# Optimization experiments

Measured on AMD Instinct MI355X. Metric: run time of the kernel, lower is better.

Reference implementation:

```python
import jax, jax.numpy as jnp
import numpy as np

N, K, H, E, HEADS, MULT = 10000, 32, 128, 128, 8, 2
HD = H // HEADS


def _ln(x, g, b):
    m = jnp.mean(x, axis=-1, keepdims=True)
    v = jnp.var(x, axis=-1, keepdims=True)
    return (x - m) * jax.lax.rsqrt(v + 1e-5) * g + b


def setup_inputs() -> dict:
    key = jax.random.key(0)
    ks = jax.random.split(key, 40)
    s = 0.05
    inp = {
        "node_features": jax.random.normal(ks[0], (N, H), jnp.float32),
        "edge_features": jax.random.normal(ks[1], (N, K, H), jnp.float32),
        "edge_attr": jax.random.normal(ks[2], (N, K, E), jnp.float32),
        "neighbor_list": jax.random.randint(ks[3], (N, K), 0, N),
        "num_valid": jax.random.randint(ks[4], (N,), 1, K + 1),
        # edge_linear: E -> H (with activation)
        "W_edge": jax.random.normal(ks[5], (E, H), jnp.float32) * s,
        "b_edge": jnp.zeros((H,), jnp.float32),
        # node_linear: 2H -> H (cat of center + gathered neighbor features)
        "W_node": jax.random.normal(ks[6], (2 * H, H), jnp.float32) * s,
        "b_node": jnp.zeros((H,), jnp.float32),
        # message_linear: 2H -> H
        "W_msg": jax.random.normal(ks[7], (2 * H, H), jnp.float32) * s,
        "b_msg": jnp.zeros((H,), jnp.float32),
        # multi-head attention in/out projections
        "W_qkv": jax.random.normal(ks[8], (H, 3 * H), jnp.float32) * s,
        "b_qkv": jnp.zeros((3 * H,), jnp.float32),
        "W_out": jax.random.normal(ks[9], (H, H), jnp.float32) * s,
        "b_out": jnp.zeros((H,), jnp.float32),
        # layernorms
        "g_attn": jnp.ones((H,), jnp.float32), "be_attn": jnp.zeros((H,), jnp.float32),
        "g_fn": jnp.ones((H,), jnp.float32), "be_fn": jnp.zeros((H,), jnp.float32),
        "g_fe": jnp.ones((H,), jnp.float32), "be_fe": jnp.zeros((H,), jnp.float32),
        # FFNs (node and edge), hidden = MULT*H
        "Wn1": jax.random.normal(ks[10], (H, MULT * H), jnp.float32) * s,
        "bn1": jnp.zeros((MULT * H,), jnp.float32),
        "Wn2": jax.random.normal(ks[11], (MULT * H, H), jnp.float32) * s,
        "bn2": jnp.zeros((H,), jnp.float32),
        "We1": jax.random.normal(ks[12], (H, MULT * H), jnp.float32) * s,
        "be1": jnp.zeros((MULT * H,), jnp.float32),
        "We2": jax.random.normal(ks[13], (MULT * H, H), jnp.float32) * s,
        "be2": jnp.zeros((H,), jnp.float32),
    }
    return inp


def _block(node_features, edge_features, edge_attr, neighbor_list, mask,
           W_edge, b_edge, W_node, b_node, W_msg, b_msg,
           W_qkv, b_qkv, W_out, b_out,
           g_attn, be_attn, g_fn, be_fn, g_fe, be_fe,
           Wn1, bn1, Wn2, bn2, We1, be1, We2, be2):
    act = jax.nn.gelu
    # --- pre-attention norm on nodes ---
    node_hidden = _ln(node_features, g_attn, be_attn)                 # [N,H]
    # --- graph attention: gather -> MLPs -> local windowed attention -> scatter ---
    edge_hidden = act(jnp.einsum('nke,eh->nkh', edge_attr, W_edge) + b_edge)   # [N,K,H]
    nbr = node_hidden[neighbor_list]                                   # [N,K,H] gather
    center = jnp.broadcast_to(node_hidden[:, None, :], nbr.shape)      # [N,K,H]
    node_cat = jnp.concatenate([center, nbr], axis=-1)                 # [N,K,2H]
    node_hid = act(jnp.einsum('nkf,fh->nkh', node_cat, W_node) + b_node)
    msg = act(jnp.einsum('nkf,fh->nkh',
                         jnp.concatenate([edge_hidden, node_hid], axis=-1),
                         W_msg) + b_msg)                               # [N,K,H]
    # multi-head self-attention per node over its K neighbors, key padding mask
    qkv = jnp.einsum('nkh,hf->nkf', msg, W_qkv) + b_qkv                # [N,K,3H]
    q, k, v = jnp.split(qkv, 3, axis=-1)
    q = q.reshape(N, K, HEADS, HD)
    k = k.reshape(N, K, HEADS, HD)
    v = v.reshape(N, K, HEADS, HD)
    scores = jnp.einsum('nqhd,nkhd->nhqk', q, k) / np.sqrt(HD)         # [N,heads,K,K]
    scores = jnp.where(mask[:, None, None, :], scores, jnp.float32(-1e9))
    attn = jax.nn.softmax(scores, axis=-1)
    ctx = jnp.einsum('nhqk,nkhd->nqhd', attn, v).reshape(N, K, H)
    edge_out = jnp.einsum('nkh,hf->nkf', ctx, W_out) + b_out           # [N,K,H]
    # masked scatter-aggregate back to nodes
    node_out = jnp.sum(edge_out * mask[:, :, None], axis=1)            # [N,H]
    # residuals
    node_features = node_out + node_features
    edge_features = edge_out + edge_features
    # --- FFN block ---
    nh = _ln(node_features, g_fn, be_fn)
    eh = _ln(edge_features, g_fe, be_fe)
    nh = act(nh @ Wn1 + bn1) @ Wn2 + bn2
    eh = jnp.einsum('nkf,fh->nkh', act(jnp.einsum('nkh,hf->nkf', eh, We1) + be1), We2) + be2
    return node_features + nh, edge_features + eh


def reference(node_features, edge_features, edge_attr, neighbor_list, num_valid,
              W_edge, b_edge, W_node, b_node, W_msg, b_msg,
              W_qkv, b_qkv, W_out, b_out,
              g_attn, be_attn, g_fn, be_fn, g_fe, be_fe,
              Wn1, bn1, Wn2, bn2, We1, be1, We2, be2):
    mask = jnp.arange(K)[None, :] < num_valid[:, None]                 # [N,K] bool
    return _block(node_features, edge_features, edge_attr, neighbor_list, mask,
                  W_edge, b_edge, W_node, b_node, W_msg, b_msg,
                  W_qkv, b_qkv, W_out, b_out,
                  g_attn, be_attn, g_fn, be_fn, g_fe, be_fe,
                  Wn1, bn1, Wn2, bn2, We1, be1, We2, be2)
```

## Files before the change

kernel.cpp:

```cpp
#include <hip/hip_runtime.h>
#include <hip/hip_bf16.h>
#include <cstddef>

#define N_NODES 10000
#define KNBR 32
#define HDIM 128
#define NHEADS 8

using short8 = __attribute__((ext_vector_type(8))) short;
using short4v = __attribute__((ext_vector_type(4))) short;
using f32x4 = __attribute__((ext_vector_type(4))) float;

__device__ __forceinline__ f32x4 mfma16(short8 a, short8 b, f32x4 c) {
  return __builtin_amdgcn_mfma_f32_16x16x32_bf16(a, b, c, 0, 0, 0);
}

__device__ __forceinline__ short f2bf(float f) {
  __hip_bfloat16 h = __float2bfloat16(f);
  return __builtin_bit_cast(short, h);
}
__device__ __forceinline__ float bf2f(short s) {
  unsigned u = ((unsigned)(unsigned short)s) << 16;
  return __builtin_bit_cast(float, u);
}

__device__ __forceinline__ float gelu_f(float x) {
  float u = x * fmaf(x * x, -0.1029432f, -2.3022077f);
  return x * __builtin_amdgcn_rcpf(1.0f + __builtin_amdgcn_exp2f(u));
}

__device__ __forceinline__ short4v pack4f(float a, float b, float c, float d) {
  short4v v; v[0] = f2bf(a); v[1] = f2bf(b); v[2] = f2bf(c); v[3] = f2bf(d);
  return v;
}
__device__ __forceinline__ short4v pack_gelu4(f32x4 acc, float4 bb) {
  return pack4f(gelu_f(acc[0] + bb.x), gelu_f(acc[1] + bb.y),
                gelu_f(acc[2] + bb.z), gelu_f(acc[3] + bb.w));
}

__device__ __forceinline__ short8 ld_sw128(const short* b, int r, int ch) {
  return *(const short8*)(b + r * 128 + (((ch ^ (r & 7))) << 3));
}
__device__ __forceinline__ short8 ld_sw256(const short* b, int r, int ch) {
  return *(const short8*)(b + r * 256 + (((ch ^ (r & 7))) << 3));
}
__device__ __forceinline__ void st_sw128(short* b, int r, int col, short v) {
  b[r * 128 + ((((col >> 3) ^ (r & 7))) << 3) + (col & 7)] = v;
}
__device__ __forceinline__ void st_sw128_v4(short* b, int r, int colb, short4v v) {
  *(short4v*)(b + r * 128 + ((((colb >> 3) ^ (r & 7))) << 3) + (colb & 7)) = v;
}
__device__ __forceinline__ void st_sw256_v4(short* b, int r, int colb, short4v v) {
  *(short4v*)(b + r * 256 + ((((colb >> 3) ^ (r & 7))) << 3) + (colb & 7)) = v;
}


template <int MT, int NT, int KS, typename ALoad, typename Epi>
__device__ __forceinline__ void wgemm(ALoad aload, const short* __restrict__ Bt,
                                      Epi epi) {
  const int lane = threadIdx.x & 63;
  const int lm = lane & 15, lq = lane >> 4;
#pragma unroll
  for (int nt = 0; nt < NT; ++nt) {
    short8 b[KS];
#pragma unroll
    for (int k = 0; k < KS; ++k)
      b[k] = *(const short8*)(Bt + (nt * 16 + lm) * (KS * 32) + k * 32 + lq * 8);
#pragma unroll
    for (int mt = 0; mt < MT; ++mt) {
      short8 a[KS];
#pragma unroll
      for (int k = 0; k < KS; ++k) a[k] = aload(mt * 16 + lm, k, lq);
      f32x4 acc = {0.f, 0.f, 0.f, 0.f};
#pragma unroll
      for (int k = 0; k < KS; ++k) acc = mfma16(a[k], b[k], acc);
      epi(mt, nt, acc);
    }
  }
}

template <int MT, int NT, int KS, typename ALoad, typename Epi>
__device__ __forceinline__ void wgemm_t(ALoad aload, const short* __restrict__ Bt,
                                        Epi epi) {
  const int lane = threadIdx.x & 63;
  const int lm = lane & 15, lq = lane >> 4;
#pragma unroll
  for (int nt = 0; nt < NT; ++nt) {
    short8 b[KS];
#pragma unroll
    for (int k = 0; k < KS; ++k)
      b[k] = *(const short8*)(Bt + (nt * 16 + lm) * (KS * 32) + k * 32 + lq * 8);
#pragma unroll
    for (int mt = 0; mt < MT; ++mt) {
      short8 a[KS];
#pragma unroll
      for (int k = 0; k < KS; ++k) a[k] = aload(mt * 16 + lm, k, lq);
      f32x4 acc = {0.f, 0.f, 0.f, 0.f};
#pragma unroll
      for (int k = 0; k < KS; ++k) acc = mfma16(b[k], a[k], acc);
      epi(mt, nt, acc);
    }
  }
}

template <int MT, int NT, int KS, typename ALoad>
__device__ __forceinline__ void wgemm_pass(ALoad aload,
                                           const short* __restrict__ Bt,
                                           int brs, f32x4 (&acc)[MT][NT]) {
  const int lane = threadIdx.x & 63;
  const int lm = lane & 15, lq = lane >> 4;
#pragma unroll
  for (int nt = 0; nt < NT; ++nt) {
    short8 b[KS];
#pragma unroll
    for (int k = 0; k < KS; ++k)
      b[k] = *(const short8*)(Bt + (nt * 16 + lm) * brs + k * 32 + lq * 8);
#pragma unroll
    for (int mt = 0; mt < MT; ++mt) {
      short8 a[KS];
#pragma unroll
      for (int k = 0; k < KS; ++k) a[k] = aload(mt * 16 + lm, k, lq);
#pragma unroll
      for (int k = 0; k < KS; ++k)
        acc[mt][nt] = mfma16(a[k], b[k], acc[mt][nt]);
    }
  }
}

template <int MT, int NT, int KS, typename ALoad>
__device__ __forceinline__ void wgemm_t_pass(ALoad aload,
                                             const short* __restrict__ Bt,
                                             int brs, f32x4 (&acc)[MT][NT]) {
  const int lane = threadIdx.x & 63;
  const int lm = lane & 15, lq = lane >> 4;
#pragma unroll
  for (int nt = 0; nt < NT; ++nt) {
    short8 b[KS];
#pragma unroll
    for (int k = 0; k < KS; ++k)
      b[k] = *(const short8*)(Bt + (nt * 16 + lm) * brs + k * 32 + lq * 8);
#pragma unroll
    for (int mt = 0; mt < MT; ++mt) {
      short8 a[KS];
#pragma unroll
      for (int k = 0; k < KS; ++k) a[k] = aload(mt * 16 + lm, k, lq);
#pragma unroll
      for (int k = 0; k < KS; ++k)
        acc[mt][nt] = mfma16(b[k], a[k], acc[mt][nt]);
    }
  }
}

struct WSrc { const float* p[9]; };

__global__ void wprep_kernel(WSrc ws, short* __restrict__ dst) {
  const int cum[10] = {0, 16384, 49152, 81920, 131072, 147456, 180224, 212992, 245760, 278528};
  const int Ks[9] = {128, 256, 256, 128, 128, 128, 256, 128, 256};
  const int Ns[9] = {128, 128, 128, 384, 128, 256, 128, 256, 128};
  int eg = blockIdx.x * 256 + threadIdx.x;
  int id = 0;
#pragma unroll
  for (int i = 0; i < 8; ++i) id += (eg >= cum[i + 1]) ? 1 : 0;
  int e = eg - cum[id];
  int K = Ks[id];
  int n = (K == 128) ? (e >> 7) : (e >> 8);
  int k = e - n * K;
  dst[eg] = f2bf(ws.p[id][k * Ns[id] + n]);
}

__global__ __launch_bounds__(256) void ln_in_kernel(
    const float* __restrict__ in, const float* __restrict__ g,
    const float* __restrict__ be, short* __restrict__ out) {
  __shared__ float scr[32 * 8 * 2 + 64];
  const int tid = threadIdx.x;
  const int r = tid >> 3, j = tid & 7;
  const int base = blockIdx.x * 32;
  const int rg = base + r;
  const bool valid = rg < N_NODES;
  float4 v[4];
#pragma unroll
  for (int i = 0; i < 4; ++i)
    v[i] = valid ? ((const float4*)(in + (size_t)rg * 128 + j * 16))[i]
                 : make_float4(0.f, 0.f, 0.f, 0.f);
  float s = 0.f, s2 = 0.f;
#pragma unroll
  for (int i = 0; i < 4; ++i) {
    s += v[i].x + v[i].y + v[i].z + v[i].w;
    s2 = fmaf(v[i].x, v[i].x, s2); s2 = fmaf(v[i].y, v[i].y, s2);
    s2 = fmaf(v[i].z, v[i].z, s2); s2 = fmaf(v[i].w, v[i].w, s2);
  }
  scr[r * 8 + j] = s;
  scr[256 + r * 8 + j] = s2;
  __syncthreads();
  if (tid < 32) {
    float ss = 0.f, q2 = 0.f;
#pragma unroll
    for (int i = 0; i < 8; ++i) { ss += scr[tid * 8 + i]; q2 += scr[256 + tid * 8 + i]; }
    float mn = ss * (1.f / 128.f);
    float vr = fmaf(-mn, mn, q2 * (1.f / 128.f));
    scr[512 + tid] = mn;
    scr[544 + tid] = rsqrtf(vr + 1e-5f);
  }
  __syncthreads();
  if (!valid) return;
  float mn = scr[512 + r], rs = scr[544 + r];
  short8 o[2];
#pragma unroll
  for (int i = 0; i < 4; ++i) {
    int c0 = j * 16 + i * 4;
    float4 gg = *(const float4*)(g + c0);
    float4 bb = *(const float4*)(be + c0);
    float* vf = (float*)&v[i];
    float* gf = (float*)&gg;
    float* bf = (float*)&bb;
#pragma unroll
    for (int e = 0; e < 4; ++e)
      o[i >> 1][(i & 1) * 4 + e] = f2bf(fmaf((vf[e] - mn) * rs, gf[e], bf[e]));
  }
  *(short8*)(out + (size_t)rg * 128 + j * 16) = o[0];
  *(short8*)(out + (size_t)rg * 128 + j * 16 + 8) = o[1];
}

__global__ __launch_bounds__(256, 4) void egab_main(
    const float* __restrict__ nf, const float* __restrict__ ef,
    const float* __restrict__ ea, const int* __restrict__ nlist,
    const int* __restrict__ nvalid,
    const float* __restrict__ b_edge, const float* __restrict__ b_node,
    const float* __restrict__ b_msg, const float* __restrict__ b_qkv,
    const float* __restrict__ b_out, const float* __restrict__ g_fe,
    const float* __restrict__ be_fe, const float* __restrict__ be1,
    const float* __restrict__ be2,
    const short* __restrict__ WtE, const short* __restrict__ WtN,
    const short* __restrict__ WtM, const short* __restrict__ WtQ,
    const short* __restrict__ WtO, const short* __restrict__ WtE1,
    const short* __restrict__ WtE2, const short* __restrict__ nh_bf,
    float* __restrict__ out_node, float* __restrict__ out_edge) {
  __shared__ short lds[16384];
  short* R0 = lds;
  short* R1 = lds + 4096;
  short* R2 = lds + 8192;
  short* R3 = lds + 12288;

  const int tid = threadIdx.x;
  const int w = tid >> 6;
  const int lane = tid & 63;
  const int lm = lane & 15, lq = lane >> 4;
  const int base = blockIdx.x;
  const int n0 = w * 32;

  {
    const float* eap = ea + (size_t)base * 4096;
    int r = tid >> 3;
    int sg = tid & 7;
#pragma unroll
    for (int j = 0; j < 2; ++j) {
      int ch = sg * 2 + j;
      float4 fa = ((const float4*)eap)[r * 32 + ch * 2];
      float4 fb = ((const float4*)eap)[r * 32 + ch * 2 + 1];
      short8 v = {f2bf(fa.x), f2bf(fa.y), f2bf(fa.z), f2bf(fa.w),
                  f2bf(fb.x), f2bf(fb.y), f2bf(fb.z), f2bf(fb.w)};
      *(short8*)(R0 + r * 128 + ((ch ^ (r & 7)) << 3)) = v;
    }
    int idx = nlist[base * KNBR + r];
    const short* srow = nh_bf + (size_t)idx * 128;
#pragma unroll
    for (int j = 0; j < 2; ++j) {
      int ch = sg * 2 + j;
      short8 v = *(const short8*)(srow + ch * 8);
      *(short8*)(R1 + r * 128 + ((ch ^ (r & 7)) << 3)) = v;
    }
  }
  __syncthreads();

  wgemm_t<2, 2, 4>(
      [&](int r, int k, int q) { return ld_sw128(R0, r, k * 4 + q); },
      WtE + (size_t)n0 * 128,
      [&](int mt, int nt, f32x4 acc) {
        int colb = n0 + nt * 16 + lq * 4;
        float4 bb = *(const float4*)(b_edge + colb);
        st_sw128_v4(R2, mt * 16 + lm, colb, pack_gelu4(acc, bb));
      });
  {
    f32x4 ac[2][2];
#pragma unroll
    for (int mt = 0; mt < 2; ++mt)
#pragma unroll
      for (int nt = 0; nt < 2; ++nt) ac[mt][nt] = {0.f, 0.f, 0.f, 0.f};
    wgemm_t_pass<2, 2, 4>(
        [&](int r, int k, int q) {
          (void)r;
          return *(const short8*)(nh_bf + (size_t)base * 128 + k * 32 + q * 8);
        },
        WtN + (size_t)n0 * 256, 256, ac);
    wgemm_t_pass<2, 2, 4>(
        [&](int r, int k, int q) { return ld_sw128(R1, r, k * 4 + q); },
        WtN + (size_t)n0 * 256 + 128, 256, ac);
#pragma unroll
    for (int mt = 0; mt < 2; ++mt)
#pragma unroll
      for (int nt = 0; nt < 2; ++nt) {
        int colb = n0 + nt * 16 + lq * 4;
        float4 bb = *(const float4*)(b_node + colb);
        st_sw128_v4(R3, mt * 16 + lm, colb, pack_gelu4(ac[mt][nt], bb));
      }
  }
  __syncthreads();

  {
    f32x4 ac[2][2];
#pragma unroll
    for (int mt = 0; mt < 2; ++mt)
#pragma unroll
      for (int nt = 0; nt < 2; ++nt) ac[mt][nt] = {0.f, 0.f, 0.f, 0.f};
    wgemm_t_pass<2, 2, 4>(
        [&](int r, int k, int q) { return ld_sw128(R2, r, k * 4 + q); },
        WtM + (size_t)n0 * 256, 256, ac);
    wgemm_t_pass<2, 2, 4>(
        [&](int r, int k, int q) { return ld_sw128(R3, r, k * 4 + q); },
        WtM + (size_t)n0 * 256 + 128, 256, ac);
#pragma unroll
    for (int mt = 0; mt < 2; ++mt)
#pragma unroll
      for (int nt = 0; nt < 2; ++nt) {
        int colb = n0 + nt * 16 + lq * 4;
        float4 bb = *(const float4*)(b_msg + colb);
        st_sw128_v4(R0, mt * 16 + lm, colb, pack_gelu4(ac[mt][nt], bb));
      }
  }
  __syncthreads();

  {
    const int q0 = w * 96;
    wgemm<2, 6, 4>(
        [&](int r, int k, int q) { return ld_sw128(R0, r, k * 4 + q); },
        WtQ + (size_t)q0 * 128,
        [&](int mt, int nt, f32x4 acc) {
          int c = q0 + nt * 16;
          float bb = b_qkv[c + lm];
          int m = mt * 16 + lq * 4;
          if (c < 256) {
            short* dst = (c < 128 ? R1 + ((c >> 4) * 32) * 16
                                  : R2 + (((c - 128) >> 4) * 32) * 16);
#pragma unroll
            for (int rr = 0; rr < 4; ++rr)
              dst[(m + rr) * 16 + lm] = f2bf(acc[rr] + bb);
          } else {
            int rv = (c - 256) + lm;
            short4v pv;
#pragma unroll
            for (int rr = 0; rr < 4; ++rr) pv[rr] = f2bf(acc[rr] + bb);
            int chv = m >> 3;
            *(short4v*)(R3 + rv * 32 + ((chv ^ (rv & 3)) << 3) + (m & 7)) = pv;
          }
        });
  }
  __syncthreads();

  {
    const short8 zz = {0, 0, 0, 0, 0, 0, 0, 0};
    const f32x4 z4 = {0.f, 0.f, 0.f, 0.f};
    const int nvv = nvalid[base];
#pragma unroll
    for (int it = 0; it < 2; ++it) {
      int h = (it << 2) | w;
      short* qh = R1 + h * 512;
      short* kh = R2 + h * 512;
      short8 bk[2];
#pragma unroll
      for (int nt = 0; nt < 2; ++nt)
        bk[nt] = (lq < 2) ? *(const short8*)(kh + (nt * 16 + lm) * 16 + lq * 8) : zz;
      float sc[2][2][4];
#pragma unroll
      for (int mt = 0; mt < 2; ++mt) {
        short8 aq = (lq < 2) ? *(const short8*)(qh + (mt * 16 + lm) * 16 + lq * 8) : zz;
#pragma unroll
        for (int nt = 0; nt < 2; ++nt) {
          f32x4 s = mfma16(aq, bk[nt], z4);
#pragma unroll
          for (int rr = 0; rr < 4; ++rr) {
            float x = s[rr] * 0.25f;
            if (nt * 16 + lm >= nvv) x = -1e9f;
            sc[mt][nt][rr] = x;
          }
        }
      }
#pragma unroll
      for (int mt = 0; mt < 2; ++mt)
#pragma unroll
        for (int rr = 0; rr < 4; ++rr) {
          float x0 = sc[mt][0][rr], x1 = sc[mt][1][rr];
          float mx = fmaxf(x0, x1);
          mx = fmaxf(mx, __shfl_xor(mx, 1, 16));
          mx = fmaxf(mx, __shfl_xor(mx, 2, 16));
          mx = fmaxf(mx, __shfl_xor(mx, 4, 16));
          mx = fmaxf(mx, __shfl_xor(mx, 8, 16));
          float e0 = __expf(x0 - mx), e1 = __expf(x1 - mx);
          float sm = e0 + e1;
          sm += __shfl_xor(sm, 1, 16);
          sm += __shfl_xor(sm, 2, 16);
          sm += __shfl_xor(sm, 4, 16);
          sm += __shfl_xor(sm, 8, 16);
          float ri = 1.f / sm;
          int row = mt * 16 + lq * 4 + rr;
          qh[row * 16 + lm] = f2bf(e0 * ri);
          kh[row * 16 + lm] = f2bf(e1 * ri);
        }
#pragma unroll
      for (int mt = 0; mt < 2; ++mt) {
        const short* psrc = (lq < 2) ? qh : kh;
        short8 pa = *(const short8*)(psrc + (mt * 16 + lm) * 16 + (lq & 1) * 8);
        int rv = h * 16 + lm;
        short8 vb = *(const short8*)(R3 + rv * 32 + ((lq ^ (rv & 3)) << 3));
        f32x4 c = mfma16(pa, vb, z4);
#pragma unroll
        for (int rr = 0; rr < 4; ++rr)
          st_sw128(R0, mt * 16 + lq * 4 + rr, h * 16 + lm, f2bf(c[rr]));
      }
    }
  }
  __syncthreads();

  {
    int nv = nvalid[base];
    float nsum[2] = {0.f, 0.f};
    wgemm<2, 2, 4>(
        [&](int r, int k, int q) { return ld_sw128(R0, r, k * 4 + q); },
        WtO + (size_t)n0 * 128,
        [&](int mt, int nt, f32x4 acc) {
          int col = n0 + nt * 16 + lm;
          float bb = b_out[col];
#pragma unroll
          for (int rr = 0; rr < 4; ++rr) {
            int kk = mt * 16 + lq * 4 + rr;
            float eo = acc[rr] + bb;
            if (kk < nv) nsum[nt] += eo;
            float efv = ef[((size_t)base * KNBR + kk) * 128 + col];
            st_sw128(R1, kk, col, f2bf(eo + efv));
          }
        });
#pragma unroll
    for (int nt = 0; nt < 2; ++nt) {
      float v = nsum[nt];
      v += __shfl_xor(v, 16, 64);
      v += __shfl_xor(v, 32, 64);
      if (lq == 0) {
        int col = n0 + nt * 16 + lm;
        out_node[(size_t)base * 128 + col] =
            v + nf[(size_t)base * 128 + col];
      }
    }
  }
  __syncthreads();

  {
    float* scr = (float*)R2;
    int r = tid >> 3, sg = tid & 7;
    short8 xv[2];
    float s = 0.f, s2 = 0.f;
#pragma unroll
    for (int j = 0; j < 2; ++j) {
      int ch = sg * 2 + j;
      xv[j] = *(const short8*)(R1 + r * 128 + ((ch ^ (r & 7)) << 3));
#pragma unroll
      for (int e = 0; e < 8; ++e) {
        float x = bf2f(xv[j][e]);
        s += x;
        s2 = fmaf(x, x, s2);
      }
    }
    scr[r * 8 + sg] = s;
    scr[256 + r * 8 + sg] = s2;
    __syncthreads();
    if (tid < 32) {
      float ss = 0.f, q2 = 0.f;
#pragma unroll
      for (int i = 0; i < 8; ++i) { ss += scr[tid * 8 + i]; q2 += scr[256 + tid * 8 + i]; }
      float mn = ss * (1.f / 128.f);
      float vr = fmaf(-mn, mn, q2 * (1.f / 128.f));
      scr[512 + tid * 2] = mn;
      scr[512 + tid * 2 + 1] = rsqrtf(vr + 1e-5f);
    }
    __syncthreads();
    float mn = scr[512 + r * 2], rs = scr[512 + r * 2 + 1];
#pragma unroll
    for (int j = 0; j < 2; ++j) {
      int ch = sg * 2 + j;
      int c0 = ch * 8;
      float4 g0 = *(const float4*)(g_fe + c0);
      float4 g1 = *(const float4*)(g_fe + c0 + 4);
      float4 b0 = *(const float4*)(be_fe + c0);
      float4 b1 = *(const float4*)(be_fe + c0 + 4);
      const float* gp0 = (const float*)&g0;
      const float* gp1 = (const float*)&g1;
      const float* bp0 = (const float*)&b0;
      const float* bp1 = (const float*)&b1;
      short8 ov;
#pragma unroll
      for (int e = 0; e < 4; ++e) {
        ov[e] = f2bf(fmaf((bf2f(xv[j][e]) - mn) * rs, gp0[e], bp0[e]));
        ov[4 + e] = f2bf(fmaf((bf2f(xv[j][4 + e]) - mn) * rs, gp1[e], bp1[e]));
      }
      *(short8*)(R0 + r * 128 + ((ch ^ (r & 7)) << 3)) = ov;
    }
  }
  __syncthreads();

  {
    const int f0 = w * 64;
    wgemm_t<2, 4, 4>(
        [&](int r, int k, int q) { return ld_sw128(R0, r, k * 4 + q); },
        WtE1 + (size_t)f0 * 128,
        [&](int mt, int nt, f32x4 acc) {
          int colb = f0 + nt * 16 + lq * 4;
          float4 bb = *(const float4*)(be1 + colb);
          st_sw256_v4(R2, mt * 16 + lm, colb, pack_gelu4(acc, bb));
        });
  }
  __syncthreads();

  {
    f32x4 ac[2][2];
#pragma unroll
    for (int mt = 0; mt < 2; ++mt)
#pragma unroll
      for (int nt = 0; nt < 2; ++nt) ac[mt][nt] = {0.f, 0.f, 0.f, 0.f};
    wgemm_pass<2, 2, 4>(
        [&](int r, int k, int q) { return ld_sw256(R2, r, k * 4 + q); },
        WtE2 + (size_t)n0 * 256, 256, ac);
    wgemm_pass<2, 2, 4>(
        [&](int r, int k, int q) { return ld_sw256(R2, r, 16 + k * 4 + q); },
        WtE2 + (size_t)n0 * 256 + 128, 256, ac);
#pragma unroll
    for (int mt = 0; mt < 2; ++mt)
#pragma unroll
      for (int nt = 0; nt < 2; ++nt) {
        int col = n0 + nt * 16 + lm;
        float bb = be2[col];
#pragma unroll
        for (int rr = 0; rr < 4; ++rr) {
          int m = mt * 16 + lq * 4 + rr;
          float rv = bf2f(R1[m * 128 + ((((col >> 3) ^ (m & 7))) << 3) + (col & 7)]);
          out_edge[((size_t)base * KNBR + m) * 128 + col] =
              rv + ac[mt][nt][rr] + bb;
        }
      }
  }
}

__global__ __launch_bounds__(256, 4) void node_ffn_kernel(
    const float* __restrict__ nres, const float* __restrict__ g,
    const float* __restrict__ be, const short* __restrict__ WtN1,
    const float* __restrict__ bn1, const short* __restrict__ WtN2,
    const float* __restrict__ bn2, float* __restrict__ out) {
  __shared__ short lds[8192];
  short* EHN = lds;
  float* scr = (float*)(lds + 2048);
  short* HID = lds + 4096;

  const int tid = threadIdx.x;
  const int w = tid >> 6;
  const int lane = tid & 63;
  const int lm = lane & 15, lq = lane >> 4;
  const int base = blockIdx.x * 16;
  const int n0 = w * 32;

  {
    int r = tid >> 4, sg = tid & 15;
    bool valid = (base + r) < N_NODES;
    float xf[8];
#pragma unroll
    for (int i = 0; i < 2; ++i) {
      float4 v = valid ? ((const float4*)(nres + (size_t)(base + r) * 128 + sg * 8))[i]
                       : make_float4(0.f, 0.f, 0.f, 0.f);
      xf[i * 4] = v.x; xf[i * 4 + 1] = v.y; xf[i * 4 + 2] = v.z; xf[i * 4 + 3] = v.w;
    }
    float s = 0.f, s2 = 0.f;
#pragma unroll
    for (int i = 0; i < 8; ++i) { s += xf[i]; s2 = fmaf(xf[i], xf[i], s2); }
    scr[r * 16 + sg] = s;
    scr[256 + r * 16 + sg] = s2;
    __syncthreads();
    if (tid < 16) {
      float ss = 0.f, q2 = 0.f;
#pragma unroll
      for (int i = 0; i < 16; ++i) { ss += scr[tid * 16 + i]; q2 += scr[256 + tid * 16 + i]; }
      float mn = ss * (1.f / 128.f);
      float vr = fmaf(-mn, mn, q2 * (1.f / 128.f));
      scr[512 + tid * 2] = mn;
      scr[512 + tid * 2 + 1] = rsqrtf(vr + 1e-5f);
    }
    __syncthreads();
    float mn = scr[512 + r * 2], rs = scr[512 + r * 2 + 1];
    int c0 = sg * 8;
    short8 ov;
#pragma unroll
    for (int e = 0; e < 8; ++e)
      ov[e] = f2bf(fmaf((xf[e] - mn) * rs, g[c0 + e], be[c0 + e]));
    *(short8*)(EHN + r * 128 + ((sg ^ (r & 7)) << 3)) = ov;
  }
  __syncthreads();

  {
    const int f0 = w * 64;
    wgemm_t<1, 4, 4>(
        [&](int r, int k, int q) { return ld_sw128(EHN, r, k * 4 + q); },
        WtN1 + (size_t)f0 * 128,
        [&](int mt, int nt, f32x4 acc) {
          int colb = f0 + nt * 16 + lq * 4;
          float4 bb = *(const float4*)(bn1 + colb);
          st_sw256_v4(HID, mt * 16 + lm, colb, pack_gelu4(acc, bb));
        });
  }
  __syncthreads();

  {
    f32x4 ac[1][2];
    ac[0][0] = {0.f, 0.f, 0.f, 0.f};
    ac[0][1] = {0.f, 0.f, 0.f, 0.f};
    wgemm_pass<1, 2, 4>(
        [&](int r, int k, int q) { return ld_sw256(HID, r, k * 4 + q); },
        WtN2 + (size_t)n0 * 256, 256, ac);
    wgemm_pass<1, 2, 4>(
        [&](int r, int k, int q) { return ld_sw256(HID, r, 16 + k * 4 + q); },
        WtN2 + (size_t)n0 * 256 + 128, 256, ac);
#pragma unroll
    for (int nt = 0; nt < 2; ++nt) {
      int col = n0 + nt * 16 + lm;
      float bb = bn2[col];
#pragma unroll
      for (int rr = 0; rr < 4; ++rr) {
        int m = lq * 4 + rr;
        if (base + m < N_NODES) {
          float rv = nres[(size_t)(base + m) * 128 + col];
          out[(size_t)(base + m) * 128 + col] = rv + ac[0][nt][rr] + bb;
        }
      }
    }
  }
}

extern "C" void kernel_launch(void* const* d_in, const int* in_sizes, int n_in,
                              void* d_out, int out_size, void* d_ws,
                              size_t ws_size, hipStream_t stream) {
  (void)in_sizes; (void)n_in; (void)out_size; (void)ws_size;
  const float* nf = (const float*)d_in[0];
  const float* ef = (const float*)d_in[1];
  const float* ea = (const float*)d_in[2];
  const int* nlist = (const int*)d_in[3];
  const int* nvalid = (const int*)d_in[4];
  const float* W_edge = (const float*)d_in[5];
  const float* b_edge = (const float*)d_in[6];
  const float* W_node = (const float*)d_in[7];
  const float* b_node = (const float*)d_in[8];
  const float* W_msg = (const float*)d_in[9];
  const float* b_msg = (const float*)d_in[10];
  const float* W_qkv = (const float*)d_in[11];
  const float* b_qkv = (const float*)d_in[12];
  const float* W_out = (const float*)d_in[13];
  const float* b_out = (const float*)d_in[14];
  const float* g_attn = (const float*)d_in[15];
  const float* be_attn = (const float*)d_in[16];
  const float* g_fn = (const float*)d_in[17];
  const float* be_fn = (const float*)d_in[18];
  const float* g_fe = (const float*)d_in[19];
  const float* be_fe = (const float*)d_in[20];
  const float* Wn1 = (const float*)d_in[21];
  const float* bn1 = (const float*)d_in[22];
  const float* Wn2 = (const float*)d_in[23];
  const float* bn2 = (const float*)d_in[24];
  const float* We1 = (const float*)d_in[25];
  const float* be1 = (const float*)d_in[26];
  const float* We2 = (const float*)d_in[27];
  const float* be2 = (const float*)d_in[28];

  short* ws0 = (short*)d_ws;
  short* wsW = ws0 + 1280000;
  short* WtE = wsW;
  short* WtN = wsW + 16384;
  short* WtM = wsW + 49152;
  short* WtQ = wsW + 81920;
  short* WtO = wsW + 131072;
  short* WtE1 = wsW + 147456;
  short* WtE2 = wsW + 180224;
  short* WtN1 = wsW + 212992;
  short* WtN2 = wsW + 245760;

  float* out_node = (float*)d_out;
  float* out_edge = out_node + (size_t)N_NODES * 128;

  WSrc wsrc;
  wsrc.p[0] = W_edge; wsrc.p[1] = W_node; wsrc.p[2] = W_msg;
  wsrc.p[3] = W_qkv;  wsrc.p[4] = W_out;  wsrc.p[5] = We1;
  wsrc.p[6] = We2;    wsrc.p[7] = Wn1;    wsrc.p[8] = Wn2;

  wprep_kernel<<<1088, 256, 0, stream>>>(wsrc, wsW);
  ln_in_kernel<<<(N_NODES + 31) / 32, 256, 0, stream>>>(nf, g_attn, be_attn, ws0);
  egab_main<<<N_NODES, 256, 0, stream>>>(
      nf, ef, ea, nlist, nvalid, b_edge, b_node, b_msg, b_qkv, b_out, g_fe,
      be_fe, be1, be2, WtE, WtN, WtM, WtQ, WtO, WtE1, WtE2, ws0, out_node,
      out_edge);
  node_ffn_kernel<<<(N_NODES + 15) / 16, 256, 0, stream>>>(
      out_node, g_fn, be_fn, WtN1, bn1, WtN2, bn2, out_node);
}
```

Before: 892.0 us.

## Repartition edge-kernel GEMM tiles so each wave owns one row block

Changes the per-wave work split in the fused edge kernel. Before, each of 4 waves covered all 32 edge rows and a 32-column slice. Now each wave covers 16 rows and a wider column slice, so A fragments are loaded from LDS once and reused across all N tiles, while B (weight) fragments are reloaded for each row half. The node-sum reduction now goes through an LDS partial-sum buffer plus an extra sync to combine the two row halves. The trade is fewer LDS A loads against more global or L2 weight loads and one additional barrier.

```diff
diff --git a/kernel.cpp b/kernel.cpp
--- a/kernel.cpp
+++ b/kernel.cpp
@@ -55,60 +55,57 @@
 }
 
 
-template <int MT, int NT, int KS, typename ALoad, typename Epi>
-__device__ __forceinline__ void wgemm(ALoad aload, const short* __restrict__ Bt,
-                                      Epi epi) {
+template <int NT, int KS, typename ALoad, typename Epi>
+__device__ __forceinline__ void wgemm1(int rb, ALoad aload,
+                                       const short* __restrict__ Bt, Epi epi) {
   const int lane = threadIdx.x & 63;
   const int lm = lane & 15, lq = lane >> 4;
+  short8 a[KS];
+#pragma unroll
+  for (int k = 0; k < KS; ++k) a[k] = aload(rb + lm, k, lq);
 #pragma unroll
   for (int nt = 0; nt < NT; ++nt) {
     short8 b[KS];
 #pragma unroll
     for (int k = 0; k < KS; ++k)
       b[k] = *(const short8*)(Bt + (nt * 16 + lm) * (KS * 32) + k * 32 + lq * 8);
-#pragma unroll
-    for (int mt = 0; mt < MT; ++mt) {
-      short8 a[KS];
-#pragma unroll
-      for (int k = 0; k < KS; ++k) a[k] = aload(mt * 16 + lm, k, lq);
-      f32x4 acc = {0.f, 0.f, 0.f, 0.f};
-#pragma unroll
-      for (int k = 0; k < KS; ++k) acc = mfma16(a[k], b[k], acc);
-      epi(mt, nt, acc);
-    }
-  }
-}
-
-template <int MT, int NT, int KS, typename ALoad, typename Epi>
-__device__ __forceinline__ void wgemm_t(ALoad aload, const short* __restrict__ Bt,
-                                        Epi epi) {
+    f32x4 acc = {0.f, 0.f, 0.f, 0.f};
+#pragma unroll
+    for (int k = 0; k < KS; ++k) acc = mfma16(a[k], b[k], acc);
+    epi(nt, acc);
+  }
+}
+
+template <int NT, int KS, typename ALoad, typename Epi>
+__device__ __forceinline__ void wgemm1_t(int rb, ALoad aload,
+                                         const short* __restrict__ Bt, Epi epi) {
   const int lane = threadIdx.x & 63;
   const int lm = lane & 15, lq = lane >> 4;
+  short8 a[KS];
+#pragma unroll
+  for (int k = 0; k < KS; ++k) a[k] = aload(rb + lm, k, lq);
 #pragma unroll
   for (int nt = 0; nt < NT; ++nt) {
     short8 b[KS];
 #pragma unroll
     for (int k = 0; k < KS; ++k)
       b[k] = *(const short8*)(Bt + (nt * 16 + lm) * (KS * 32) + k * 32 + lq * 8);
-#pragma unroll
-    for (int mt = 0; mt < MT; ++mt) {
-      short8 a[KS];
-#pragma unroll
-      for (int k = 0; k < KS; ++k) a[k] = aload(mt * 16 + lm, k, lq);
-      f32x4 acc = {0.f, 0.f, 0.f, 0.f};
-#pragma unroll
-      for (int k = 0; k < KS; ++k) acc = mfma16(b[k], a[k], acc);
-      epi(mt, nt, acc);
-    }
-  }
-}
-
-template <int MT, int NT, int KS, typename ALoad>
-__device__ __forceinline__ void wgemm_pass(ALoad aload,
-                                           const short* __restrict__ Bt,
-                                           int brs, f32x4 (&acc)[MT][NT]) {
+    f32x4 acc = {0.f, 0.f, 0.f, 0.f};
+#pragma unroll
+    for (int k = 0; k < KS; ++k) acc = mfma16(b[k], a[k], acc);
+    epi(nt, acc);
+  }
+}
+
+template <int NT, int KS, typename ALoad>
+__device__ __forceinline__ void wgemm1_pass(int rb, ALoad aload,
+                                            const short* __restrict__ Bt,
+                                            int brs, f32x4 (&acc)[NT]) {
   const int lane = threadIdx.x & 63;
   const int lm = lane & 15, lq = lane >> 4;
+  short8 a[KS];
+#pragma unroll
+  for (int k = 0; k < KS; ++k) a[k] = aload(rb + lm, k, lq);
 #pragma unroll
   for (int nt = 0; nt < NT; ++nt) {
     short8 b[KS];
@@ -116,23 +113,19 @@
     for (int k = 0; k < KS; ++k)
       b[k] = *(const short8*)(Bt + (nt * 16 + lm) * brs + k * 32 + lq * 8);
 #pragma unroll
-    for (int mt = 0; mt < MT; ++mt) {
-      short8 a[KS];
-#pragma unroll
-      for (int k = 0; k < KS; ++k) a[k] = aload(mt * 16 + lm, k, lq);
-#pragma unroll
-      for (int k = 0; k < KS; ++k)
-        acc[mt][nt] = mfma16(a[k], b[k], acc[mt][nt]);
-    }
-  }
-}
-
-template <int MT, int NT, int KS, typename ALoad>
-__device__ __forceinline__ void wgemm_t_pass(ALoad aload,
-                                             const short* __restrict__ Bt,
-                                             int brs, f32x4 (&acc)[MT][NT]) {
+    for (int k = 0; k < KS; ++k) acc[nt] = mfma16(a[k], b[k], acc[nt]);
+  }
+}
+
+template <int NT, int KS, typename ALoad>
+__device__ __forceinline__ void wgemm1_t_pass(int rb, ALoad aload,
+                                              const short* __restrict__ Bt,
+                                              int brs, f32x4 (&acc)[NT]) {
   const int lane = threadIdx.x & 63;
   const int lm = lane & 15, lq = lane >> 4;
+  short8 a[KS];
+#pragma unroll
+  for (int k = 0; k < KS; ++k) a[k] = aload(rb + lm, k, lq);
 #pragma unroll
   for (int nt = 0; nt < NT; ++nt) {
     short8 b[KS];
@@ -140,14 +133,7 @@
     for (int k = 0; k < KS; ++k)
       b[k] = *(const short8*)(Bt + (nt * 16 + lm) * brs + k * 32 + lq * 8);
 #pragma unroll
-    for (int mt = 0; mt < MT; ++mt) {
-      short8 a[KS];
-#pragma unroll
-      for (int k = 0; k < KS; ++k) a[k] = aload(mt * 16 + lm, k, lq);
-#pragma unroll
-      for (int k = 0; k < KS; ++k)
-        acc[mt][nt] = mfma16(b[k], a[k], acc[mt][nt]);
-    }
+    for (int k = 0; k < KS; ++k) acc[nt] = mfma16(b[k], a[k], acc[nt]);
   }
 }
 
@@ -246,7 +232,9 @@
   const int lane = tid & 63;
   const int lm = lane & 15, lq = lane >> 4;
   const int base = blockIdx.x;
-  const int n0 = w * 32;
+  const int hw = w & 1;
+  const int cw = w >> 1;
+  const int rb = hw * 16;
 
   {
     const float* eap = ea + (size_t)base * 4096;
@@ -272,72 +260,67 @@
   }
   __syncthreads();
 
-  wgemm_t<2, 2, 4>(
-      [&](int r, int k, int q) { return ld_sw128(R0, r, k * 4 + q); },
-      WtE + (size_t)n0 * 128,
-      [&](int mt, int nt, f32x4 acc) {
-        int colb = n0 + nt * 16 + lq * 4;
-        float4 bb = *(const float4*)(b_edge + colb);
-        st_sw128_v4(R2, mt * 16 + lm, colb, pack_gelu4(acc, bb));
-      });
-  {
-    f32x4 ac[2][2];
-#pragma unroll
-    for (int mt = 0; mt < 2; ++mt)
-#pragma unroll
-      for (int nt = 0; nt < 2; ++nt) ac[mt][nt] = {0.f, 0.f, 0.f, 0.f};
-    wgemm_t_pass<2, 2, 4>(
+  {
+    const int c0 = cw * 64;
+    wgemm1_t<4, 4>(
+        rb, [&](int r, int k, int q) { return ld_sw128(R0, r, k * 4 + q); },
+        WtE + (size_t)c0 * 128,
+        [&](int nt, f32x4 acc) {
+          int colb = c0 + nt * 16 + lq * 4;
+          float4 bb = *(const float4*)(b_edge + colb);
+          st_sw128_v4(R2, rb + lm, colb, pack_gelu4(acc, bb));
+        });
+    f32x4 ac[4];
+#pragma unroll
+    for (int nt = 0; nt < 4; ++nt) ac[nt] = {0.f, 0.f, 0.f, 0.f};
+    wgemm1_t_pass<4, 4>(
+        rb,
         [&](int r, int k, int q) {
           (void)r;
           return *(const short8*)(nh_bf + (size_t)base * 128 + k * 32 + q * 8);
         },
-        WtN + (size_t)n0 * 256, 256, ac);
-    wgemm_t_pass<2, 2, 4>(
-        [&](int r, int k, int q) { return ld_sw128(R1, r, k * 4 + q); },
-        WtN + (size_t)n0 * 256 + 128, 256, ac);
-#pragma unroll
-    for (int mt = 0; mt < 2; ++mt)
-#pragma unroll
-      for (int nt = 0; nt < 2; ++nt) {
-        int colb = n0 + nt * 16 + lq * 4;
-        float4 bb = *(const float4*)(b_node + colb);
-        st_sw128_v4(R3, mt * 16 + lm, colb, pack_gelu4(ac[mt][nt], bb));
-      }
-  }
-  __syncthreads();
-
-  {
-    f32x4 ac[2][2];
-#pragma unroll
-    for (int mt = 0; mt < 2; ++mt)
-#pragma unroll
-      for (int nt = 0; nt < 2; ++nt) ac[mt][nt] = {0.f, 0.f, 0.f, 0.f};
-    wgemm_t_pass<2, 2, 4>(
-        [&](int r, int k, int q) { return ld_sw128(R2, r, k * 4 + q); },
-        WtM + (size_t)n0 * 256, 256, ac);
-    wgemm_t_pass<2, 2, 4>(
-        [&](int r, int k, int q) { return ld_sw128(R3, r, k * 4 + q); },
-        WtM + (size_t)n0 * 256 + 128, 256, ac);
-#pragma unroll
-    for (int mt = 0; mt < 2; ++mt)
-#pragma unroll
-      for (int nt = 0; nt < 2; ++nt) {
-        int colb = n0 + nt * 16 + lq * 4;
-        float4 bb = *(const float4*)(b_msg + colb);
-        st_sw128_v4(R0, mt * 16 + lm, colb, pack_gelu4(ac[mt][nt], bb));
-      }
-  }
-  __syncthreads();
-
-  {
-    const int q0 = w * 96;
-    wgemm<2, 6, 4>(
-        [&](int r, int k, int q) { return ld_sw128(R0, r, k * 4 + q); },
-        WtQ + (size_t)q0 * 128,
-        [&](int mt, int nt, f32x4 acc) {
-          int c = q0 + nt * 16;
+        WtN + (size_t)c0 * 256, 256, ac);
+    wgemm1_t_pass<4, 4>(
+        rb, [&](int r, int k, int q) { return ld_sw128(R1, r, k * 4 + q); },
+        WtN + (size_t)c0 * 256 + 128, 256, ac);
+#pragma unroll
+    for (int nt = 0; nt < 4; ++nt) {
+      int colb = c0 + nt * 16 + lq * 4;
+      float4 bb = *(const float4*)(b_node + colb);
+      st_sw128_v4(R3, rb + lm, colb, pack_gelu4(ac[nt], bb));
+    }
+  }
+  __syncthreads();
+
+  {
+    const int c0 = cw * 64;
+    f32x4 ac[4];
+#pragma unroll
+    for (int nt = 0; nt < 4; ++nt) ac[nt] = {0.f, 0.f, 0.f, 0.f};
+    wgemm1_t_pass<4, 4>(
+        rb, [&](int r, int k, int q) { return ld_sw128(R2, r, k * 4 + q); },
+        WtM + (size_t)c0 * 256, 256, ac);
+    wgemm1_t_pass<4, 4>(
+        rb, [&](int r, int k, int q) { return ld_sw128(R3, r, k * 4 + q); },
+        WtM + (size_t)c0 * 256 + 128, 256, ac);
+#pragma unroll
+    for (int nt = 0; nt < 4; ++nt) {
+      int colb = c0 + nt * 16 + lq * 4;
+      float4 bb = *(const float4*)(b_msg + colb);
+      st_sw128_v4(R0, rb + lm, colb, pack_gelu4(ac[nt], bb));
+    }
+  }
+  __syncthreads();
+
+  {
+    const int c0 = cw * 192;
+    wgemm1<12, 4>(
+        rb, [&](int r, int k, int q) { return ld_sw128(R0, r, k * 4 + q); },
+        WtQ + (size_t)c0 * 128,
+        [&](int nt, f32x4 acc) {
+          int c = c0 + nt * 16;
           float bb = b_qkv[c + lm];
-          int m = mt * 16 + lq * 4;
+          int m = rb + lq * 4;
           if (c < 256) {
             short* dst = (c < 128 ? R1 + ((c >> 4) * 32) * 16
                                   : R2 + (((c - 128) >> 4) * 32) * 16);
@@ -421,38 +404,40 @@
   __syncthreads();
 
   {
+    const int c0 = cw * 64;
     int nv = nvalid[base];
-    float nsum[2] = {0.f, 0.f};
-    wgemm<2, 2, 4>(
-        [&](int r, int k, int q) { return ld_sw128(R0, r, k * 4 + q); },
-        WtO + (size_t)n0 * 128,
-        [&](int mt, int nt, f32x4 acc) {
-          int col = n0 + nt * 16 + lm;
+    float nsum[4] = {0.f, 0.f, 0.f, 0.f};
+    wgemm1<4, 4>(
+        rb, [&](int r, int k, int q) { return ld_sw128(R0, r, k * 4 + q); },
+        WtO + (size_t)c0 * 128,
+        [&](int nt, f32x4 acc) {
+          int col = c0 + nt * 16 + lm;
           float bb = b_out[col];
 #pragma unroll
           for (int rr = 0; rr < 4; ++rr) {
-            int kk = mt * 16 + lq * 4 + rr;
+            int kk = rb + lq * 4 + rr;
             float eo = acc[rr] + bb;
             if (kk < nv) nsum[nt] += eo;
             float efv = ef[((size_t)base * KNBR + kk) * 128 + col];
             st_sw128(R1, kk, col, f2bf(eo + efv));
           }
         });
-#pragma unroll
-    for (int nt = 0; nt < 2; ++nt) {
+    float* ps = (float*)R3;
+#pragma unroll
+    for (int nt = 0; nt < 4; ++nt) {
       float v = nsum[nt];
       v += __shfl_xor(v, 16, 64);
       v += __shfl_xor(v, 32, 64);
-      if (lq == 0) {
-        int col = n0 + nt * 16 + lm;
-        out_node[(size_t)base * 128 + col] =
-            v + nf[(size_t)base * 128 + col];
-      }
-    }
-  }
-  __syncthreads();
-
-  {
+      if (lq == 0) ps[hw * 128 + c0 + nt * 16 + lm] = v;
+    }
+  }
+  __syncthreads();
+
+  {
+    float* ps = (float*)R3;
+    if (tid < 128)
+      out_node[(size_t)base * 128 + tid] =
+          ps[tid] + ps[128 + tid] + nf[(size_t)base * 128 + tid];
     float* scr = (float*)R2;
     int r = tid >> 3, sg = tid & 7;
     short8 xv[2];
@@ -506,44 +491,40 @@
   __syncthreads();
 
   {
-    const int f0 = w * 64;
-    wgemm_t<2, 4, 4>(
-        [&](int r, int k, int q) { return ld_sw128(R0, r, k * 4 + q); },
-        WtE1 + (size_t)f0 * 128,
-        [&](int mt, int nt, f32x4 acc) {
-          int colb = f0 + nt * 16 + lq * 4;
+    const int c0 = cw * 128;
+    wgemm1_t<8, 4>(
+        rb, [&](int r, int k, int q) { return ld_sw128(R0, r, k * 4 + q); },
+        WtE1 + (size_t)c0 * 128,
+        [&](int nt, f32x4 acc) {
+          int colb = c0 + nt * 16 + lq * 4;
           float4 bb = *(const float4*)(be1 + colb);
-          st_sw256_v4(R2, mt * 16 + lm, colb, pack_gelu4(acc, bb));
+          st_sw256_v4(R2, rb + lm, colb, pack_gelu4(acc, bb));
         });
   }
   __syncthreads();
 
   {
-    f32x4 ac[2][2];
-#pragma unroll
-    for (int mt = 0; mt < 2; ++mt)
-#pragma unroll
-      for (int nt = 0; nt < 2; ++nt) ac[mt][nt] = {0.f, 0.f, 0.f, 0.f};
-    wgemm_pass<2, 2, 4>(
-        [&](int r, int k, int q) { return ld_sw256(R2, r, k * 4 + q); },
-        WtE2 + (size_t)n0 * 256, 256, ac);
-    wgemm_pass<2, 2, 4>(
-        [&](int r, int k, int q) { return ld_sw256(R2, r, 16 + k * 4 + q); },
-        WtE2 + (size_t)n0 * 256 + 128, 256, ac);
-#pragma unroll
-    for (int mt = 0; mt < 2; ++mt)
-#pragma unroll
-      for (int nt = 0; nt < 2; ++nt) {
-        int col = n0 + nt * 16 + lm;
-        float bb = be2[col];
-#pragma unroll
-        for (int rr = 0; rr < 4; ++rr) {
-          int m = mt * 16 + lq * 4 + rr;
-          float rv = bf2f(R1[m * 128 + ((((col >> 3) ^ (m & 7))) << 3) + (col & 7)]);
-          out_edge[((size_t)base * KNBR + m) * 128 + col] =
-              rv + ac[mt][nt][rr] + bb;
-        }
+    const int c0 = cw * 64;
+    f32x4 ac[4];
+#pragma unroll
+    for (int nt = 0; nt < 4; ++nt) ac[nt] = {0.f, 0.f, 0.f, 0.f};
+    wgemm1_pass<4, 4>(
+        rb, [&](int r, int k, int q) { return ld_sw256(R2, r, k * 4 + q); },
+        WtE2 + (size_t)c0 * 256, 256, ac);
+    wgemm1_pass<4, 4>(
+        rb, [&](int r, int k, int q) { return ld_sw256(R2, r, 16 + k * 4 + q); },
+        WtE2 + (size_t)c0 * 256 + 128, 256, ac);
+#pragma unroll
+    for (int nt = 0; nt < 4; ++nt) {
+      int col = c0 + nt * 16 + lm;
+      float bb = be2[col];
+#pragma unroll
+      for (int rr = 0; rr < 4; ++rr) {
+        int m = rb + lq * 4 + rr;
+        float rv = bf2f(R1[m * 128 + ((((col >> 3) ^ (m & 7))) << 3) + (col & 7)]);
+        out_edge[((size_t)base * KNBR + m) * 128 + col] = rv + ac[nt][rr] + bb;
       }
+    }
   }
 }
 
@@ -602,26 +583,26 @@
 
   {
     const int f0 = w * 64;
-    wgemm_t<1, 4, 4>(
-        [&](int r, int k, int q) { return ld_sw128(EHN, r, k * 4 + q); },
+    wgemm1_t<4, 4>(
+        0, [&](int r, int k, int q) { return ld_sw128(EHN, r, k * 4 + q); },
         WtN1 + (size_t)f0 * 128,
-        [&](int mt, int nt, f32x4 acc) {
+        [&](int nt, f32x4 acc) {
           int colb = f0 + nt * 16 + lq * 4;
           float4 bb = *(const float4*)(bn1 + colb);
-          st_sw256_v4(HID, mt * 16 + lm, colb, pack_gelu4(acc, bb));
+          st_sw256_v4(HID, lm, colb, pack_gelu4(acc, bb));
         });
   }
   __syncthreads();
 
   {
-    f32x4 ac[1][2];
-    ac[0][0] = {0.f, 0.f, 0.f, 0.f};
-    ac[0][1] = {0.f, 0.f, 0.f, 0.f};
-    wgemm_pass<1, 2, 4>(
-        [&](int r, int k, int q) { return ld_sw256(HID, r, k * 4 + q); },
+    f32x4 ac[2];
+    ac[0] = {0.f, 0.f, 0.f, 0.f};
+    ac[1] = {0.f, 0.f, 0.f, 0.f};
+    wgemm1_pass<2, 4>(
+        0, [&](int r, int k, int q) { return ld_sw256(HID, r, k * 4 + q); },
         WtN2 + (size_t)n0 * 256, 256, ac);
-    wgemm_pass<1, 2, 4>(
-        [&](int r, int k, int q) { return ld_sw256(HID, r, 16 + k * 4 + q); },
+    wgemm1_pass<2, 4>(
+        0, [&](int r, int k, int q) { return ld_sw256(HID, r, 16 + k * 4 + q); },
         WtN2 + (size_t)n0 * 256 + 128, 256, ac);
 #pragma unroll
     for (int nt = 0; nt < 2; ++nt) {
@@ -632,7 +613,7 @@
         int m = lq * 4 + rr;
         if (base + m < N_NODES) {
           float rv = nres[(size_t)(base + m) * 128 + col];
-          out[(size_t)(base + m) * 128 + col] = rv + ac[0][nt][rr] + bb;
+          out[(size_t)(base + m) * 128 + col] = rv + ac[nt][rr] + bb;
         }
       }
     }
```

New measurement: 1.377 ms. 54.4% more time.
